# Kernel tuning notes

Hardware: AMD Instinct MI355X
Metric: run time of the kernel (lower is better)

The kernel has to match this reference:

```python
import jax, jax.numpy as jnp
import numpy as np

N_HEAD = 4
HIDDEN = 1024
D_HEAD = HIDDEN // N_HEAD  # 256
SEQ = 1024
BATCH = 16
NEG_INF = -1e9


def setup_inputs() -> dict:
    key = jax.random.key(0)
    k1, k2, k3 = jax.random.split(key, 3)
    x = jax.random.normal(k1, (BATCH, SEQ, HIDDEN), dtype=jnp.float32)
    # torch Linear(hidden, (2n+1)*d_head, bias=False); stored here as [in, out]
    w_qkv = jax.random.normal(k2, (HIDDEN, (2 * N_HEAD + 1) * D_HEAD), dtype=jnp.float32) * (HIDDEN ** -0.5)
    # out_proj: Linear(d_head, hidden, bias=False), stored as [d_head, hidden]
    w_out = jax.random.normal(k3, (D_HEAD, HIDDEN), dtype=jnp.float32) * (D_HEAD ** -0.5)
    return {"x": x, "w_qkv": w_qkv, "w_out": w_out}


def reference(x, w_qkv, w_out):
    bs, t, h = x.shape
    n_head, d_head = N_HEAD, D_HEAD
    scale = d_head ** -0.5
    qkv = x @ w_qkv  # [bs, t, (2n+1)*d]
    q = qkv[..., : n_head * d_head].reshape(bs, t, n_head, d_head)
    k = qkv[..., n_head * d_head : 2 * n_head * d_head].reshape(bs, t, n_head, d_head)
    v = qkv[..., 2 * n_head * d_head :]  # [bs, t, d] -- single shared V
    # scores [bs, n_head, t, s]
    scores = jnp.einsum("btnd,bsnd->bnts", q, k) * scale
    causal = jnp.triu(jnp.ones((t, t), dtype=bool), 1)  # True above diag
    scores = jnp.where(causal, NEG_INF, scores)
    attn_prob = jax.nn.softmax(scores, axis=-1)  # [bs, n_head, t, s]
    attn_vec = jnp.einsum("bnts,bsd->bntd", attn_prob, v)
    m_attn_vec = jnp.mean(attn_vec, axis=1)  # mean over heads -> [bs, t, d]
    out = m_attn_vec @ w_out  # [bs, t, hidden]
    return out, attn_prob
```

## Files before the change

### kernel.cpp

```cpp
#include <hip/hip_runtime.h>
#include <hip/hip_bf16.h>
#include <type_traits>

#define BATCH  16
#define SEQ    1024
#define HIDDEN 1024
#define NHEAD  4
#define DHEAD  256
#define QKVN   2304

typedef _Float16 f16x8 __attribute__((ext_vector_type(8)));
typedef float    f32x4 __attribute__((ext_vector_type(4)));

__device__ __forceinline__ void gll16(const void* g, void* l) {
  __builtin_amdgcn_global_load_lds(
      (const __attribute__((address_space(1))) unsigned int*)g,
      (__attribute__((address_space(3))) unsigned int*)l, 16, 0, 0);
}

__global__ __launch_bounds__(256) void f32_to_f16(
    const float* __restrict__ in, _Float16* __restrict__ out) {
  int i4 = blockIdx.x * 256 + threadIdx.x;
  float4 v = ((const float4*)in)[i4];
  _Float16 h4[4] = {(_Float16)v.x, (_Float16)v.y, (_Float16)v.z, (_Float16)v.w};
  *(uint2*)&out[(size_t)i4 * 4] = *(uint2*)h4;
}

__global__ __launch_bounds__(256) void transpose_to_f16(
    const float* __restrict__ in, _Float16* __restrict__ out, int R, int C) {
  __shared__ float tile[64][65];
  int bc = blockIdx.x * 64, br = blockIdx.y * 64;
  int t = threadIdx.x;
  int tr = t >> 6, tc = t & 63;
  for (int i = 0; i < 64; i += 4)
    tile[tr + i][tc] = in[(size_t)(br + tr + i) * C + bc + tc];
  __syncthreads();
  for (int i = 0; i < 64; i += 4)
    out[(size_t)(bc + tr + i) * R + br + tc] = (_Float16)tile[tc][tr + i];
}

__global__ __launch_bounds__(256) void transpose_v(
    const _Float16* __restrict__ qkv, _Float16* __restrict__ vT) {
  __shared__ _Float16 tile[64][65];
  int b = blockIdx.z;
  int s0 = blockIdx.x * 64, d0 = blockIdx.y * 64;
  int t = threadIdx.x;
  int tr = t >> 6, tc = t & 63;
  for (int i = 0; i < 64; i += 4)
    tile[tr + i][tc] = qkv[((size_t)(b * SEQ + s0 + tr + i)) * QKVN + 2 * NHEAD * DHEAD + d0 + tc];
  __syncthreads();
  for (int i = 0; i < 64; i += 4)
    vT[((size_t)(b * DHEAD + d0 + tr + i)) * SEQ + s0 + tc] = tile[tc][tr + i];
}

template <typename OT>
__global__ __launch_bounds__(256) void gemm_bt(
    const _Float16* __restrict__ A, const _Float16* __restrict__ B,
    OT* __restrict__ C, int M, int N, int K) {
  __shared__ __align__(16) _Float16 As[128][32];
  __shared__ __align__(16) _Float16 Bs[128][32];
  int bm = blockIdx.x * 128, bn = blockIdx.y * 128;
  int t = threadIdx.x;
  int w = t >> 6, L = t & 63, lane15 = L & 15, quad = L >> 4;
  int wr = (w >> 1) * 64, wc = (w & 1) * 64;
  f32x4 acc[4][4] = {};
  for (int k0 = 0; k0 < K; k0 += 32) {
    __syncthreads();
    for (int r = 0; r < 2; r++) {
      int u = t + r * 256;
      int row = u >> 2, c8 = u & 3;
      gll16(&A[(size_t)(bm + row) * K + k0 + c8 * 8], &As[row][c8 * 8]);
      gll16(&B[(size_t)(bn + row) * K + k0 + c8 * 8], &Bs[row][c8 * 8]);
    }
    __syncthreads();
    f16x8 af[4], bf[4];
    for (int i = 0; i < 4; i++) af[i] = *(f16x8*)&As[wr + i * 16 + lane15][quad * 8];
    for (int j = 0; j < 4; j++) bf[j] = *(f16x8*)&Bs[wc + j * 16 + lane15][quad * 8];
    for (int i = 0; i < 4; i++)
      for (int j = 0; j < 4; j++)
        acc[i][j] = __builtin_amdgcn_mfma_f32_16x16x32_f16(af[i], bf[j], acc[i][j], 0, 0, 0);
  }
  for (int i = 0; i < 4; i++)
    for (int j = 0; j < 4; j++) {
      int gr = bm + wr + i * 16 + quad * 4;
      int gc = bn + wc + j * 16 + lane15;
      for (int r = 0; r < 4; r++) {
        float v = acc[i][j][r];
        if constexpr (std::is_same_v<OT, float>)
          C[(size_t)(gr + r) * N + gc] = v;
        else
          C[(size_t)(gr + r) * N + gc] = (_Float16)v;
      }
    }
}

__global__ __launch_bounds__(512, 2) void scores_norm_kernel(
    const _Float16* __restrict__ qkv, float* __restrict__ P) {
  int lin = blockIdx.x + 16 * (blockIdx.y + 4 * blockIdx.z);
  int swz = (lin & 7) * 128 + (lin >> 3);
  int ti = swz & 15, n = (swz >> 4) & 3, b = swz >> 6;
  __shared__ __align__(16) _Float16 Qs[8][64][32];
  __shared__ __align__(16) _Float16 Ks[2][8][64][32];
  int t = threadIdx.x;
  int w = t >> 6, L = t & 63, lane15 = L & 15, quad = L >> 4;
  int r16 = (w & 3) * 16;
  int ch  = (w >> 2) * 32;
  for (int r = 0; r < 4; r++) {
    int u = t + r * 512;
    int kc = u >> 8, row = (u & 255) >> 2, c8 = u & 3;
    gll16(&qkv[((size_t)(b * SEQ + ti * 64 + row)) * QKVN + n * DHEAD + kc * 32 + c8 * 8],
          &Qs[kc][row][c8 * 8]);
    gll16(&qkv[((size_t)(b * SEQ + row)) * QKVN + NHEAD * DHEAD + n * DHEAD + kc * 32 + c8 * 8],
          &Ks[0][kc][row][c8 * 8]);
  }
  __syncthreads();
  f16x8 aq[8];
#pragma unroll
  for (int kc = 0; kc < 8; kc++) aq[kc] = *(f16x8*)&Qs[kc][r16 + lane15][quad * 8];
  f32x4 s[16][2];
  int trow = ti * 64 + r16 + quad * 4;
  const float scale = 0.0625f;
#pragma unroll
  for (int si = 0; si < 16; si++) {
    if (si <= ti) {
      if (si < ti) {
        for (int r = 0; r < 4; r++) {
          int u = t + r * 512;
          int kc = u >> 8, row = (u & 255) >> 2, c8 = u & 3;
          gll16(&qkv[((size_t)(b * SEQ + (si + 1) * 64 + row)) * QKVN + NHEAD * DHEAD + n * DHEAD + kc * 32 + c8 * 8],
                &Ks[(si + 1) & 1][kc][row][c8 * 8]);
        }
      }
      s[si][0] = (f32x4){0.f, 0.f, 0.f, 0.f};
      s[si][1] = (f32x4){0.f, 0.f, 0.f, 0.f};
      for (int kc = 0; kc < 8; kc++) {
        for (int j = 0; j < 2; j++) {
          f16x8 bk = *(f16x8*)&Ks[si & 1][kc][ch + j * 16 + lane15][quad * 8];
          s[si][j] = __builtin_amdgcn_mfma_f32_16x16x32_f16(aq[kc], bk, s[si][j], 0, 0, 0);
        }
      }
      __syncthreads();
    }
  }
  float m[4], l[4];
#pragma unroll
  for (int r = 0; r < 4; r++) {
    float mx = -INFINITY;
#pragma unroll
    for (int si = 0; si < 16; si++) {
      if (si <= ti) {
        for (int j = 0; j < 2; j++) {
          int col = si * 64 + ch + j * 16 + lane15;
          float v = s[si][j][r] * scale;
          if (col > trow + r) v = -1e9f;
          s[si][j][r] = v;
          mx = fmaxf(mx, v);
        }
      }
    }
    for (int off = 1; off < 16; off <<= 1) mx = fmaxf(mx, __shfl_xor(mx, off, 64));
    float sum = 0.f;
#pragma unroll
    for (int si = 0; si < 16; si++) {
      if (si <= ti) {
        for (int j = 0; j < 2; j++) {
          float p = __expf(s[si][j][r] - mx);
          s[si][j][r] = p;
          sum += p;
        }
      }
    }
    for (int off = 1; off < 16; off <<= 1) sum += __shfl_xor(sum, off, 64);
    m[r] = mx; l[r] = sum;
  }
  __syncthreads();
  float* sM  = (float*)&Qs[0][0][0];
  float* sL  = sM + 128;
  float* sMc = sM + 256;
  float* sRl = sM + 320;
  if (lane15 == 0) {
    for (int r = 0; r < 4; r++) {
      sM[(w >> 2) * 64 + r16 + quad * 4 + r] = m[r];
      sL[(w >> 2) * 64 + r16 + quad * 4 + r] = l[r];
    }
  }
  __syncthreads();
  if (t < 64) {
    float m0 = sM[t], m1 = sM[64 + t], l0 = sL[t], l1 = sL[64 + t];
    float mc = fmaxf(m0, m1);
    float lc = l0 * __expf(m0 - mc) + l1 * __expf(m1 - mc);
    sMc[t] = mc;
    sRl[t] = 1.0f / lc;
  }
  __syncthreads();
  float fac[4];
  for (int r = 0; r < 4; r++) {
    int row = r16 + quad * 4 + r;
    fac[r] = __expf(m[r] - sMc[row]) * sRl[row];
  }
  size_t Pbase = ((size_t)(b * NHEAD + n)) * SEQ * SEQ;
#pragma unroll
  for (int si = 0; si < 16; si++) {
    if (si <= ti) {
      for (int j = 0; j < 2; j++) {
        int col = si * 64 + ch + j * 16 + lane15;
        for (int r = 0; r < 4; r++)
          P[Pbase + (size_t)(trow + r) * SEQ + col] = s[si][j][r] * fac[r];
      }
    }
  }
  {
    float4 z = make_float4(0.f, 0.f, 0.f, 0.f);
    int c4min = (ti + 1) * 16;
    for (int u = t; u < 16384; u += 512) {
      int row = u >> 8, c4 = u & 255;
      if (c4 >= c4min)
        *(float4*)&P[Pbase + (size_t)(ti * 64 + row) * SEQ + c4 * 4] = z;
    }
  }
}

__global__ __launch_bounds__(256) void pmean_kernel(
    const float* __restrict__ P, _Float16* __restrict__ Pmean) {
  int si = blockIdx.x, ti = blockIdx.y, b = blockIdx.z;
  if (si > ti) return;
  int t = threadIdx.x;
  int row = t >> 2, c16 = (t & 3) * 16;
  size_t tile_off = (size_t)(ti * 64 + row) * SEQ + si * 64 + c16;
  float acc[16];
  for (int i = 0; i < 16; i++) acc[i] = 0.f;
  for (int n = 0; n < 4; n++) {
    const float* p = &P[((size_t)(b * NHEAD + n)) * SEQ * SEQ + tile_off];
    for (int q = 0; q < 4; q++) {
      float4 v = *(const float4*)(p + q * 4);
      acc[q * 4 + 0] += v.x; acc[q * 4 + 1] += v.y;
      acc[q * 4 + 2] += v.z; acc[q * 4 + 3] += v.w;
    }
  }
  _Float16 h[16];
  for (int i = 0; i < 16; i++) h[i] = (_Float16)(acc[i] * 0.25f);
  _Float16* pm = &Pmean[((size_t)(b * SEQ + ti * 64 + row)) * SEQ + si * 64 + c16];
  *(uint4*)pm = *(uint4*)h;
  *(uint4*)(pm + 8) = *(uint4*)(h + 8);
}

__global__ __launch_bounds__(256) void pv_kernel(
    const _Float16* __restrict__ Pmean, const _Float16* __restrict__ vT,
    _Float16* __restrict__ mattn) {
  int lin = blockIdx.x + 16 * (blockIdx.y + 4 * blockIdx.z);
  int swz = (lin & 7) * 128 + (lin >> 3);
  int ti = swz & 15, dq = (swz >> 4) & 3, b = swz >> 6;
  __shared__ __align__(16) _Float16 Pm[2][2][64][32];
  __shared__ __align__(16) _Float16 Vs[2][2][64][32];
  int t = threadIdx.x;
  int w = t >> 6, L = t & 63, lane15 = L & 15, quad = L >> 4;
  f32x4 acc[4] = {};
  for (int r = 0; r < 2; r++) {
    int u = t + r * 256;
    int kc = u >> 8, row = (u & 255) >> 2, c8 = u & 3;
    gll16(&Pmean[((size_t)(b * SEQ + ti * 64 + row)) * SEQ + kc * 32 + c8 * 8],
          &Pm[0][kc][row][c8 * 8]);
    gll16(&vT[((size_t)(b * DHEAD + dq * 64 + row)) * SEQ + kc * 32 + c8 * 8],
          &Vs[0][kc][row][c8 * 8]);
  }
  __syncthreads();
  for (int si = 0; si <= ti; si++) {
    int cb = si & 1;
    if (si < ti) {
      for (int r = 0; r < 2; r++) {
        int u = t + r * 256;
        int kc = u >> 8, row = (u & 255) >> 2, c8 = u & 3;
        gll16(&Pmean[((size_t)(b * SEQ + ti * 64 + row)) * SEQ + (si + 1) * 64 + kc * 32 + c8 * 8],
              &Pm[cb ^ 1][kc][row][c8 * 8]);
        gll16(&vT[((size_t)(b * DHEAD + dq * 64 + row)) * SEQ + (si + 1) * 64 + kc * 32 + c8 * 8],
              &Vs[cb ^ 1][kc][row][c8 * 8]);
      }
    }
#pragma unroll
    for (int kc = 0; kc < 2; kc++) {
      f16x8 ap = *(f16x8*)&Pm[cb][kc][w * 16 + lane15][quad * 8];
#pragma unroll
      for (int j = 0; j < 4; j++) {
        f16x8 bv = *(f16x8*)&Vs[cb][kc][j * 16 + lane15][quad * 8];
        acc[j] = __builtin_amdgcn_mfma_f32_16x16x32_f16(ap, bv, acc[j], 0, 0, 0);
      }
    }
    __syncthreads();
  }
  for (int j = 0; j < 4; j++) {
    int row = b * SEQ + ti * 64 + w * 16 + quad * 4;
    int col = dq * 64 + j * 16 + lane15;
    for (int r = 0; r < 4; r++)
      mattn[(size_t)(row + r) * DHEAD + col] = (_Float16)acc[j][r];
  }
}

extern "C" void kernel_launch(void* const* d_in, const int* in_sizes, int n_in,
                              void* d_out, int out_size, void* d_ws, size_t ws_size,
                              hipStream_t stream) {
  const float* x     = (const float*)d_in[0];
  const float* w_qkv = (const float*)d_in[1];
  const float* w_out = (const float*)d_in[2];
  float* out = (float*)d_out;
  float* P   = out + (size_t)BATCH * SEQ * HIDDEN;

  _Float16* wqkvT = (_Float16*)d_ws;
  _Float16* woutT = wqkvT + (size_t)QKVN * HIDDEN;
  _Float16* qkvb  = woutT + (size_t)HIDDEN * DHEAD;
  _Float16* vT    = qkvb + (size_t)BATCH * SEQ * QKVN;
  _Float16* mattn = qkvb;
  _Float16* Pmean = qkvb + (size_t)BATCH * SEQ * DHEAD;
  _Float16* xh    = (_Float16*)P;

  f32_to_f16<<<BATCH * SEQ * HIDDEN / 1024, 256, 0, stream>>>(x, xh);
  transpose_to_f16<<<dim3(QKVN / 64, HIDDEN / 64), 256, 0, stream>>>(w_qkv, wqkvT, HIDDEN, QKVN);
  transpose_to_f16<<<dim3(HIDDEN / 64, DHEAD / 64), 256, 0, stream>>>(w_out, woutT, DHEAD, HIDDEN);
  gemm_bt<_Float16><<<dim3(BATCH * SEQ / 128, QKVN / 128), 256, 0, stream>>>(
      xh, wqkvT, qkvb, BATCH * SEQ, QKVN, HIDDEN);
  transpose_v<<<dim3(SEQ / 64, DHEAD / 64, BATCH), 256, 0, stream>>>(qkvb, vT);
  scores_norm_kernel<<<dim3(SEQ / 64, NHEAD, BATCH), 512, 0, stream>>>(qkvb, P);
  pmean_kernel<<<dim3(SEQ / 64, SEQ / 64, BATCH), 256, 0, stream>>>(P, Pmean);
  pv_kernel<<<dim3(SEQ / 64, 4, BATCH), 256, 0, stream>>>(Pmean, vT, mattn);
  gemm_bt<float><<<dim3(BATCH * SEQ / 128, HIDDEN / 128), 256, 0, stream>>>(
      mattn, woutT, out, BATCH * SEQ, HIDDEN, DHEAD);
}
```

Measured before the change: 638.9 us.

## Replace GEMMs with 256x256 double-buffered swizzled kernel and fuse V transpose

Replaces the 128x128 single-buffered GEMM with a 256x256-tile, 512-thread kernel. It uses a K-step of 64, XOR-swizzled LDS layout, double-buffered global-to-LDS prefetch interleaved with MFMA phases, and XCD-aware block remapping. The QKV projection epilogue now writes the V columns directly in transposed form, which removes the separate transpose_v launch. Trade-offs: much higher register and LDS use per block, and strided 8-byte writes for vT.

```diff
diff --git a/kernel.cpp b/kernel.cpp
--- a/kernel.cpp
+++ b/kernel.cpp
@@ -39,57 +39,111 @@
     out[(size_t)(bc + tr + i) * R + br + tc] = (_Float16)tile[tc][tr + i];
 }
 
-__global__ __launch_bounds__(256) void transpose_v(
-    const _Float16* __restrict__ qkv, _Float16* __restrict__ vT) {
-  __shared__ _Float16 tile[64][65];
-  int b = blockIdx.z;
-  int s0 = blockIdx.x * 64, d0 = blockIdx.y * 64;
-  int t = threadIdx.x;
-  int tr = t >> 6, tc = t & 63;
-  for (int i = 0; i < 64; i += 4)
-    tile[tr + i][tc] = qkv[((size_t)(b * SEQ + s0 + tr + i)) * QKVN + 2 * NHEAD * DHEAD + d0 + tc];
-  __syncthreads();
-  for (int i = 0; i < 64; i += 4)
-    vT[((size_t)(b * DHEAD + d0 + tr + i)) * SEQ + s0 + tc] = tile[tc][tr + i];
-}
-
-template <typename OT>
-__global__ __launch_bounds__(256) void gemm_bt(
+__device__ __forceinline__ void stage_chunk(
+    const _Float16* __restrict__ G, int ldg, int k0, int rowbase,
+    _Float16* ldsbase, int chunk, int t) {
+  int o16 = chunk * 512 + t;
+  int row = o16 >> 3;
+  int c = (o16 & 7) ^ (row & 7);
+  gll16(&G[(size_t)(rowbase + row) * ldg + k0 + c * 8],
+        (char*)ldsbase + (size_t)o16 * 16);
+}
+
+__device__ __forceinline__ f16x8 ldsrd(const _Float16* base, int R, int ech) {
+  int byte = R * 128 + ((ech * 16) ^ ((R & 7) << 4));
+  return *(const f16x8*)((const char*)base + byte);
+}
+
+template <typename OT, bool FUSEV>
+__global__ __launch_bounds__(512, 2) void gemm256(
     const _Float16* __restrict__ A, const _Float16* __restrict__ B,
-    OT* __restrict__ C, int M, int N, int K) {
-  __shared__ __align__(16) _Float16 As[128][32];
-  __shared__ __align__(16) _Float16 Bs[128][32];
-  int bm = blockIdx.x * 128, bn = blockIdx.y * 128;
-  int t = threadIdx.x;
-  int w = t >> 6, L = t & 63, lane15 = L & 15, quad = L >> 4;
-  int wr = (w >> 1) * 64, wc = (w & 1) * 64;
-  f32x4 acc[4][4] = {};
-  for (int k0 = 0; k0 < K; k0 += 32) {
-    __syncthreads();
-    for (int r = 0; r < 2; r++) {
-      int u = t + r * 256;
-      int row = u >> 2, c8 = u & 3;
-      gll16(&A[(size_t)(bm + row) * K + k0 + c8 * 8], &As[row][c8 * 8]);
-      gll16(&B[(size_t)(bn + row) * K + k0 + c8 * 8], &Bs[row][c8 * 8]);
-    }
-    __syncthreads();
-    f16x8 af[4], bf[4];
-    for (int i = 0; i < 4; i++) af[i] = *(f16x8*)&As[wr + i * 16 + lane15][quad * 8];
-    for (int j = 0; j < 4; j++) bf[j] = *(f16x8*)&Bs[wc + j * 16 + lane15][quad * 8];
-    for (int i = 0; i < 4; i++)
-      for (int j = 0; j < 4; j++)
-        acc[i][j] = __builtin_amdgcn_mfma_f32_16x16x32_f16(af[i], bf[j], acc[i][j], 0, 0, 0);
-  }
-  for (int i = 0; i < 4; i++)
+    OT* __restrict__ C, _Float16* __restrict__ vT, int M, int N, int K) {
+  __shared__ __align__(16) _Float16 lds[2][2][256][64];
+  int nbm = M >> 8, nbn = N >> 8;
+  int nwg = nbm * nbn;
+  int lin = blockIdx.x;
+  int q = nwg >> 3, r = nwg & 7;
+  int xcd = lin & 7, orig = lin >> 3;
+  int swz = (xcd < r ? xcd * (q + 1) : r * (q + 1) + (xcd - r) * q) + orig;
+  int bm = (swz % nbm) * 256, bn = (swz / nbm) * 256;
+  (void)nbn;
+  int t = threadIdx.x;
+  int w = t >> 6, lane = t & 63, lane15 = lane & 15, quad = lane >> 4;
+  int wm = w >> 2, wn = w & 3;
+  f32x4 acc[8][4] = {};
+  int NT = K >> 6;
+#pragma unroll
+  for (int c = 0; c < 4; c++) {
+    stage_chunk(A, K, 0, bm, &lds[0][0][0][0], c, t);
+    stage_chunk(B, K, 0, bn, &lds[0][1][0][0], c, t);
+  }
+  asm volatile("s_waitcnt vmcnt(0)" ::: "memory");
+  __builtin_amdgcn_s_barrier();
+  __builtin_amdgcn_sched_barrier(0);
+  for (int kt = 0; kt < NT; kt++) {
+    int cur = kt & 1, nxt = cur ^ 1;
+    int k1 = (kt + 1) << 6;
+    bool prefetch = (kt + 1 < NT);
+#pragma unroll
+    for (int ph = 0; ph < 4; ph++) {
+      int mh = ph >> 1, nh = ph & 1;
+      f16x8 af[2][4], bf[2][2];
+#pragma unroll
+      for (int ks = 0; ks < 2; ks++) {
+#pragma unroll
+        for (int i = 0; i < 4; i++)
+          af[ks][i] = ldsrd(&lds[cur][0][0][0],
+                            wm * 128 + (mh * 4 + i) * 16 + lane15, ks * 4 + quad);
+#pragma unroll
+        for (int j = 0; j < 2; j++)
+          bf[ks][j] = ldsrd(&lds[cur][1][0][0],
+                            wn * 64 + (nh * 2 + j) * 16 + lane15, ks * 4 + quad);
+      }
+      if (prefetch && ph < 2) {
+#pragma unroll
+        for (int c = 0; c < 2; c++) {
+          stage_chunk(A, K, k1, bm, &lds[nxt][0][0][0], ph * 2 + c, t);
+          stage_chunk(B, K, k1, bn, &lds[nxt][1][0][0], ph * 2 + c, t);
+        }
+      }
+      __builtin_amdgcn_s_barrier();
+      __builtin_amdgcn_s_setprio(1);
+#pragma unroll
+      for (int ks = 0; ks < 2; ks++)
+#pragma unroll
+        for (int i = 0; i < 4; i++)
+#pragma unroll
+          for (int j = 0; j < 2; j++)
+            acc[mh * 4 + i][nh * 2 + j] = __builtin_amdgcn_mfma_f32_16x16x32_f16(
+                af[ks][i], bf[ks][j], acc[mh * 4 + i][nh * 2 + j], 0, 0, 0);
+      __builtin_amdgcn_s_setprio(0);
+      if (ph == 3 && prefetch)
+        asm volatile("s_waitcnt vmcnt(0)" ::: "memory");
+      __builtin_amdgcn_s_barrier();
+      __builtin_amdgcn_sched_barrier(0);
+    }
+  }
+#pragma unroll
+  for (int i = 0; i < 8; i++)
+#pragma unroll
     for (int j = 0; j < 4; j++) {
-      int gr = bm + wr + i * 16 + quad * 4;
-      int gc = bn + wc + j * 16 + lane15;
-      for (int r = 0; r < 4; r++) {
-        float v = acc[i][j][r];
-        if constexpr (std::is_same_v<OT, float>)
-          C[(size_t)(gr + r) * N + gc] = v;
-        else
-          C[(size_t)(gr + r) * N + gc] = (_Float16)v;
+      int gr = bm + wm * 128 + i * 16 + quad * 4;
+      int gc = bn + wn * 64 + j * 16 + lane15;
+      bool tov = false;
+      if constexpr (FUSEV) tov = (gc >= 2 * NHEAD * DHEAD);
+      if (tov) {
+        int b = gr >> 10, s = gr & 1023, d = gc - 2 * NHEAD * DHEAD;
+        _Float16 h4[4];
+        for (int r2 = 0; r2 < 4; r2++) h4[r2] = (_Float16)acc[i][j][r2];
+        *(uint2*)&vT[((size_t)(b * DHEAD + d)) * SEQ + s] = *(uint2*)h4;
+      } else {
+        for (int r2 = 0; r2 < 4; r2++) {
+          float v = acc[i][j][r2];
+          if constexpr (std::is_same_v<OT, float>)
+            C[(size_t)(gr + r2) * N + gc] = v;
+          else
+            C[(size_t)(gr + r2) * N + gc] = (_Float16)v;
+        }
       }
     }
 }
@@ -315,12 +369,11 @@
   f32_to_f16<<<BATCH * SEQ * HIDDEN / 1024, 256, 0, stream>>>(x, xh);
   transpose_to_f16<<<dim3(QKVN / 64, HIDDEN / 64), 256, 0, stream>>>(w_qkv, wqkvT, HIDDEN, QKVN);
   transpose_to_f16<<<dim3(HIDDEN / 64, DHEAD / 64), 256, 0, stream>>>(w_out, woutT, DHEAD, HIDDEN);
-  gemm_bt<_Float16><<<dim3(BATCH * SEQ / 128, QKVN / 128), 256, 0, stream>>>(
-      xh, wqkvT, qkvb, BATCH * SEQ, QKVN, HIDDEN);
-  transpose_v<<<dim3(SEQ / 64, DHEAD / 64, BATCH), 256, 0, stream>>>(qkvb, vT);
+  gemm256<_Float16, true><<<(BATCH * SEQ / 256) * (QKVN / 256), 512, 0, stream>>>(
+      xh, wqkvT, qkvb, vT, BATCH * SEQ, QKVN, HIDDEN);
   scores_norm_kernel<<<dim3(SEQ / 64, NHEAD, BATCH), 512, 0, stream>>>(qkvb, P);
   pmean_kernel<<<dim3(SEQ / 64, SEQ / 64, BATCH), 256, 0, stream>>>(P, Pmean);
   pv_kernel<<<dim3(SEQ / 64, 4, BATCH), 256, 0, stream>>>(Pmean, vT, mattn);
-  gemm_bt<float><<<dim3(BATCH * SEQ / 128, HIDDEN / 128), 256, 0, stream>>>(
-      mattn, woutT, out, BATCH * SEQ, HIDDEN, DHEAD);
-}
+  gemm256<float, false><<<(BATCH * SEQ / 256) * (HIDDEN / 256), 512, 0, stream>>>(
+      mattn, woutT, out, nullptr, BATCH * SEQ, HIDDEN, DHEAD);
+}
```

Result: no change. 642.7 us (+0.6%).
